# Optimization experiments

Measured on AMD Instinct MI355X. Metric: run time of the kernel, lower is better.

## Reference

```python
import jax, jax.numpy as jnp
import numpy as np

N = 65536      # total voxels (lidar + image tokens)
D = 256        # d_model
H = 8          # nhead
DFF = 2048     # dim_feedforward
SS = 128       # set_size
SN = 512       # set_num (SN * SS == N, each partition is a permutation of all voxels)
NSHIFT = 2


def setup_inputs() -> dict:
    key = jax.random.key(0)
    ks = jax.random.split(key, 10)
    src = jax.random.normal(ks[0], (N, D), jnp.float32)
    pos_embed = jax.random.normal(ks[1], (NSHIFT, N, D), jnp.float32) * 0.02
    # each (shift, set_id) partition covers every voxel exactly once
    inds = jnp.stack([
        jnp.stack([
            jax.random.permutation(jax.random.fold_in(ks[2], s * 2 + p), N).reshape(SN, SS)
            for p in range(2)
        ])
        for s in range(NSHIFT)
    ]).astype(jnp.int32)                      # (NSHIFT, 2, SN, SS)
    masks = jax.random.uniform(ks[3], (NSHIFT, 2, SN, SS)) < 0.1
    masks = masks.at[..., 0].set(False)       # keep at least one key per set
    init = lambda k, shape: jax.random.normal(k, shape, jnp.float32) * 0.02
    return {
        'src': src, 'pos_embed': pos_embed,
        'set_voxel_inds': inds, 'set_voxel_masks': masks,
        'w_qkv': init(ks[4], (2, 3 * D, D)), 'b_qkv': jnp.zeros((2, 3 * D)),
        'w_out': init(ks[5], (2, D, D)), 'b_out': jnp.zeros((2, D)),
        'w_ff1': init(ks[6], (2, DFF, D)), 'b_ff1': jnp.zeros((2, DFF)),
        'w_ff2': init(ks[7], (2, D, DFF)), 'b_ff2': jnp.zeros((2, D)),
        'g_n1': jnp.ones((2, D)), 'b_n1': jnp.zeros((2, D)),
        'g_n2': jnp.ones((2, D)), 'b_n2': jnp.zeros((2, D)),
        'g_ln': jnp.ones((2, D)), 'b_ln': jnp.zeros((2, D)),
    }


def _ln(x, g, b):
    m = jnp.mean(x, -1, keepdims=True)
    v = jnp.mean(jnp.square(x - m), -1, keepdims=True)
    return (x - m) * jax.lax.rsqrt(v + 1e-5) * g + b


def _mha(q_in, k_in, v_in, mask, wqkv, bqkv, wo, bo):
    # q_in/k_in/v_in: (SN, SS, D); mask: (SN, SS) True = ignore key
    wq, wk, wv = jnp.split(wqkv, 3, axis=0)
    bq, bk, bv = jnp.split(bqkv, 3, axis=0)
    hd = D // H
    q = (q_in @ wq.T + bq).reshape(SN, SS, H, hd)
    k = (k_in @ wk.T + bk).reshape(SN, SS, H, hd)
    v = (v_in @ wv.T + bv).reshape(SN, SS, H, hd)
    scores = jnp.einsum('bqhd,bkhd->bhqk', q, k) / np.float32(np.sqrt(hd))
    scores = jnp.where(mask[:, None, None, :], jnp.float32(-1e9), scores)
    attn = jax.nn.softmax(scores, axis=-1)
    o = jnp.einsum('bhqk,bkhd->bqhd', attn, v).reshape(SN, SS, D)
    return o @ wo.T + bo


def reference(src, pos_embed, set_voxel_inds, set_voxel_masks,
              w_qkv, b_qkv, w_out, b_out, w_ff1, b_ff1, w_ff2, b_ff2,
              g_n1, b_n1, g_n2, b_n2, g_ln, b_ln):
    out = src
    set_id = 0  # block_id % 2 with block_id == 0
    for i in range(NSHIFT):  # two encoder layers, one per shift
        inds = set_voxel_inds[i, set_id]   # (SN, SS)
        mask = set_voxel_masks[i, set_id]  # (SN, SS)
        pos = pos_embed[i]
        identity = out
        feat = out[inds]                   # gather voxels into sets
        qk = feat + pos[inds]
        a = _mha(qk, qk, feat, mask, w_qkv[i], b_qkv[i], w_out[i], b_out[i])
        # scatter back: per voxel, take its FIRST occurrence in flattened set order
        flat = inds.reshape(-1)
        L = flat.shape[0]
        perm = jnp.full((N,), L, jnp.int32).at[flat].min(jnp.arange(L, dtype=jnp.int32))
        src2 = a.reshape(-1, D)[perm]
        x = _ln(out + src2, g_n1[i], b_n1[i])
        ff = jax.nn.relu(x @ w_ff1[i].T + b_ff1[i]) @ w_ff2[i].T + b_ff2[i]
        x = _ln(x + ff, g_n2[i], b_n2[i])
        out = _ln(x + identity, g_ln[i], b_ln[i])
    return out
```

## Files before the change

kernel.cpp:

```cpp
#include <hip/hip_runtime.h>
#include <math.h>

#define NVOX 65536
#define DM 256
#define NH 8
#define HDIM 32
#define DFFN 2048
#define SSZ 128
#define SNUM 512

#define AS1 __attribute__((address_space(1)))
#define AS3 __attribute__((address_space(3)))

typedef __attribute__((ext_vector_type(8))) __bf16 bf16x8;
typedef __attribute__((ext_vector_type(8))) unsigned short u16x8;
typedef __attribute__((ext_vector_type(4))) float f32x4;

__device__ __forceinline__ unsigned short f2bf(float f) {
    unsigned int u = __float_as_uint(f);
    u += 0x7fffu + ((u >> 16) & 1u);
    return (unsigned short)(u >> 16);
}
__device__ __forceinline__ float bf2f(unsigned short u) {
    return __uint_as_float(((unsigned int)u) << 16);
}

__global__ __launch_bounds__(256)
void cvt_bf16_kernel(const float* __restrict__ in, unsigned short* __restrict__ out, int n) {
    int i = blockIdx.x * 256 + threadIdx.x;
    int stride = gridDim.x * 256;
    for (; i < n; i += stride) out[i] = f2bf(in[i]);
}

__global__ __launch_bounds__(256)
void gather_kernel(const float* __restrict__ src, const float* __restrict__ pos,
                   const int* __restrict__ inds,
                   unsigned short* __restrict__ qk, unsigned short* __restrict__ feat) {
    int j = blockIdx.x * 4 + (threadIdx.x >> 6);
    int lane = threadIdx.x & 63;
    int v = inds[j];
    float4 a = ((const float4*)(src + (size_t)v * DM))[lane];
    float4 p = ((const float4*)(pos + (size_t)v * DM))[lane];
    ushort4 qo, fo;
    qo.x = f2bf(a.x + p.x); qo.y = f2bf(a.y + p.y);
    qo.z = f2bf(a.z + p.z); qo.w = f2bf(a.w + p.w);
    fo.x = f2bf(a.x); fo.y = f2bf(a.y); fo.z = f2bf(a.z); fo.w = f2bf(a.w);
    ((ushort4*)(qk   + (size_t)j * DM))[lane] = qo;
    ((ushort4*)(feat + (size_t)j * DM))[lane] = fo;
}

#define VMCNT4 asm volatile("s_waitcnt vmcnt(4)" ::: "memory")
#define VMCNT0 asm volatile("s_waitcnt vmcnt(0)" ::: "memory")

template<int EPI, bool RELU>
__global__ __launch_bounds__(512)
void gemm_mfma256(const unsigned short* __restrict__ A, const unsigned short* __restrict__ W,
                  const float* __restrict__ bias, void* __restrict__ Cout,
                  int M, int N, int K,
                  const int* __restrict__ inds,
                  const float* __restrict__ res1, const float* __restrict__ res2,
                  const float* __restrict__ g1, const float* __restrict__ b1,
                  const float* __restrict__ g2, const float* __restrict__ b2,
                  unsigned short* __restrict__ out2) {
    __shared__ alignas(16) char smem[69632];
    unsigned short* As = (unsigned short*)smem;
    unsigned short* Bs = (unsigned short*)(smem + 32768);
    float* ebuf = (float*)smem;
    const int ES = 264;

    int tid = threadIdx.x;
    int wave = tid >> 6, lane = tid & 63;
    int wm = wave >> 2;
    int wn = wave & 3;

    unsigned lin = blockIdx.x + blockIdx.y * gridDim.x;
    unsigned nwg = gridDim.x * gridDim.y;
    unsigned swz = lin;
    if ((nwg & 7u) == 0u) { unsigned cpx = nwg >> 3; swz = (lin & 7u) * cpx + (lin >> 3); }
    int bx = (int)(swz / gridDim.y);
    int by = (int)(swz % gridDim.y);
    int mBase = bx * 256, nBase = by * 256;

    int rr = lane & 15;
    int kq = (lane >> 4) * 8;
    int rbase = (lane >> 4) * 4;

    f32x4 acc[8][4];
    const f32x4 zero = {0.f, 0.f, 0.f, 0.f};
#pragma unroll
    for (int m = 0; m < 8; m++)
#pragma unroll
        for (int n = 0; n < 4; n++) acc[m][n] = zero;

    const unsigned short* gA0 = A + (size_t)(mBase + (wave * 2 + 0) * 16 + rr) * K + kq;
    const unsigned short* gA1 = A + (size_t)(mBase + (wave * 2 + 1) * 16 + rr) * K + kq;
    const unsigned short* gB0 = W + (size_t)(nBase + (wave * 2 + 0) * 16 + rr) * K + kq;
    const unsigned short* gB1 = W + (size_t)(nBase + (wave * 2 + 1) * 16 + rr) * K + kq;

    auto stage = [&](int b, int kt) {
        int ko = kt * 32;
        __builtin_amdgcn_global_load_lds((const AS1 void*)(gA0 + ko),
            (AS3 void*)(As + b * 8192 + (wave * 2 + 0) * 512), 16, 0, 0);
        __builtin_amdgcn_global_load_lds((const AS1 void*)(gA1 + ko),
            (AS3 void*)(As + b * 8192 + (wave * 2 + 1) * 512), 16, 0, 0);
        __builtin_amdgcn_global_load_lds((const AS1 void*)(gB0 + ko),
            (AS3 void*)(Bs + b * 8192 + (wave * 2 + 0) * 512), 16, 0, 0);
        __builtin_amdgcn_global_load_lds((const AS1 void*)(gB1 + ko),
            (AS3 void*)(Bs + b * 8192 + (wave * 2 + 1) * 512), 16, 0, 0);
    };

    int nt = K >> 5;
    stage(0, 0);

    for (int t = 0; t < nt; ++t) {
        int p = t & 1;
        if (t + 1 < nt) {
            stage(p ^ 1, t + 1);
            VMCNT4;
        } else {
            VMCNT0;
        }
        __builtin_amdgcn_s_barrier();
        __builtin_amdgcn_sched_barrier(0);

        bf16x8 af[8], bf[4];
#pragma unroll
        for (int m = 0; m < 8; m++)
            af[m] = *(const bf16x8*)(As + p * 8192 + (wm * 8 + m) * 512 + lane * 8);
#pragma unroll
        for (int n = 0; n < 4; n++)
            bf[n] = *(const bf16x8*)(Bs + p * 8192 + (wn * 4 + n) * 512 + lane * 8);
#pragma unroll
        for (int m = 0; m < 8; m++)
#pragma unroll
            for (int n = 0; n < 4; n++)
                acc[m][n] = __builtin_amdgcn_mfma_f32_16x16x32_bf16(af[m], bf[n], acc[m][n], 0, 0, 0);

        __builtin_amdgcn_sched_barrier(0);
        __builtin_amdgcn_s_barrier();
    }

    float bn[4];
#pragma unroll
    for (int n = 0; n < 4; n++)
        bn[n] = bias[nBase + wn * 64 + n * 16 + rr];

    int erow = tid >> 3;
    int ec0  = (tid & 7) * 32;
#pragma unroll
    for (int pass = 0; pass < 4; ++pass) {
        __syncthreads();
        if (wm == (pass >> 1)) {
#pragma unroll
            for (int mm = 0; mm < 4; ++mm) {
                int m = (pass & 1) * 4 + mm;
#pragma unroll
                for (int n = 0; n < 4; ++n) {
                    int lcol = wn * 64 + n * 16 + rr;
#pragma unroll
                    for (int r = 0; r < 4; ++r) {
                        float v = acc[m][n][r] + bn[n];
                        if (RELU) v = fmaxf(v, 0.f);
                        ebuf[(mm * 16 + rbase + r) * ES + lcol] = v;
                    }
                }
            }
        }
        __syncthreads();
        int grow = mBase + pass * 64 + erow;

        if constexpr (EPI == 0) {
            unsigned short* dst = (unsigned short*)Cout + (size_t)grow * N + nBase + ec0;
#pragma unroll
            for (int g = 0; g < 4; ++g) {
                u16x8 o;
#pragma unroll
                for (int j = 0; j < 8; ++j)
                    o[j] = f2bf(ebuf[erow * ES + ec0 + g * 8 + j]);
                *(u16x8*)(dst + g * 8) = o;
            }
        } else if constexpr (EPI == 1) {
            float* dst = (float*)Cout + (size_t)grow * N + nBase + ec0;
#pragma unroll
            for (int g = 0; g < 8; ++g)
                *(float4*)(dst + g * 4) = *(float4*)(ebuf + erow * ES + ec0 + g * 4);
        } else if constexpr (EPI == 2) {
            int v = inds[grow];
            const float* pr = res1 + (size_t)v * 256;
            f32x4 tv[8];
            float s = 0.f, s2 = 0.f;
#pragma unroll
            for (int g = 0; g < 8; ++g) {
                float4 e = *(float4*)(ebuf + erow * ES + ec0 + g * 4);
                float4 p = *(const float4*)(pr + ec0 + g * 4);
                f32x4 t = {e.x + p.x, e.y + p.y, e.z + p.z, e.w + p.w};
                tv[g] = t;
                s += t[0] + t[1] + t[2] + t[3];
                s2 += t[0]*t[0] + t[1]*t[1] + t[2]*t[2] + t[3]*t[3];
            }
#pragma unroll
            for (int off = 1; off < 8; off <<= 1) { s += __shfl_xor(s, off); s2 += __shfl_xor(s2, off); }
            float mean = s * (1.f/256.f);
            float var = fmaf(-mean, mean, s2 * (1.f/256.f));
            float rs = rsqrtf(var + 1e-5f);
            float* xd = (float*)Cout + (size_t)v * 256 + ec0;
            unsigned short* xb = out2 + (size_t)v * 256 + ec0;
#pragma unroll
            for (int g = 0; g < 8; ++g) {
                float4 gg = *(const float4*)(g1 + ec0 + g * 4);
                float4 bb = *(const float4*)(b1 + ec0 + g * 4);
                float4 o;
                o.x = fmaf((tv[g][0] - mean) * rs, gg.x, bb.x);
                o.y = fmaf((tv[g][1] - mean) * rs, gg.y, bb.y);
                o.z = fmaf((tv[g][2] - mean) * rs, gg.z, bb.z);
                o.w = fmaf((tv[g][3] - mean) * rs, gg.w, bb.w);
                *(float4*)(xd + g * 4) = o;
                ushort4 ob; ob.x = f2bf(o.x); ob.y = f2bf(o.y); ob.z = f2bf(o.z); ob.w = f2bf(o.w);
                *(ushort4*)(xb + g * 4) = ob;
            }
        } else {
            const float* xr = res2 + (size_t)grow * 256;
            const float* pr = res1 + (size_t)grow * 256;
            f32x4 tv[8];
            float s = 0.f, s2 = 0.f;
#pragma unroll
            for (int g = 0; g < 8; ++g) {
                float4 e = *(float4*)(ebuf + erow * ES + ec0 + g * 4);
                float4 x = *(const float4*)(xr + ec0 + g * 4);
                f32x4 t = {e.x + x.x, e.y + x.y, e.z + x.z, e.w + x.w};
                tv[g] = t;
                s += t[0] + t[1] + t[2] + t[3];
                s2 += t[0]*t[0] + t[1]*t[1] + t[2]*t[2] + t[3]*t[3];
            }
#pragma unroll
            for (int off = 1; off < 8; off <<= 1) { s += __shfl_xor(s, off); s2 += __shfl_xor(s2, off); }
            float mean = s * (1.f/256.f);
            float var = fmaf(-mean, mean, s2 * (1.f/256.f));
            float rs = rsqrtf(var + 1e-5f);
            float s3 = 0.f, s4 = 0.f;
#pragma unroll
            for (int g = 0; g < 8; ++g) {
                float4 gg = *(const float4*)(g1 + ec0 + g * 4);
                float4 bb = *(const float4*)(b1 + ec0 + g * 4);
                float4 p = *(const float4*)(pr + ec0 + g * 4);
                f32x4 u;
                u[0] = fmaf((tv[g][0] - mean) * rs, gg.x, bb.x) + p.x;
                u[1] = fmaf((tv[g][1] - mean) * rs, gg.y, bb.y) + p.y;
                u[2] = fmaf((tv[g][2] - mean) * rs, gg.z, bb.z) + p.z;
                u[3] = fmaf((tv[g][3] - mean) * rs, gg.w, bb.w) + p.w;
                tv[g] = u;
                s3 += u[0] + u[1] + u[2] + u[3];
                s4 += u[0]*u[0] + u[1]*u[1] + u[2]*u[2] + u[3]*u[3];
            }
#pragma unroll
            for (int off = 1; off < 8; off <<= 1) { s3 += __shfl_xor(s3, off); s4 += __shfl_xor(s4, off); }
            float mean2 = s3 * (1.f/256.f);
            float var2 = fmaf(-mean2, mean2, s4 * (1.f/256.f));
            float rs2 = rsqrtf(var2 + 1e-5f);
            float* od = (float*)Cout + (size_t)grow * 256 + ec0;
#pragma unroll
            for (int g = 0; g < 8; ++g) {
                float4 gg = *(const float4*)(g2 + ec0 + g * 4);
                float4 bb = *(const float4*)(b2 + ec0 + g * 4);
                float4 o;
                o.x = fmaf((tv[g][0] - mean2) * rs2, gg.x, bb.x);
                o.y = fmaf((tv[g][1] - mean2) * rs2, gg.y, bb.y);
                o.z = fmaf((tv[g][2] - mean2) * rs2, gg.z, bb.z);
                o.w = fmaf((tv[g][3] - mean2) * rs2, gg.w, bb.w);
                *(float4*)(od + g * 4) = o;
            }
        }
    }
}

__global__ __launch_bounds__(256)
void attn_mfma_kernel(const unsigned short* __restrict__ QK,
                      const unsigned short* __restrict__ V,
                      const unsigned char* __restrict__ mask,
                      unsigned short* __restrict__ ao) {
    int s = blockIdx.x, h = blockIdx.y;
    int tid = threadIdx.x;
    int wq = tid >> 6;
    int lane = tid & 63;

    __shared__ alignas(16) unsigned short Ks[128 * 40];
    __shared__ alignas(16) unsigned short Vt[32 * 136];
    __shared__ alignas(16) unsigned short Plds[4 * 4096];
    __shared__ unsigned char msk[SSZ];

#pragma unroll
    for (int it = 0; it < 2; it++) {
        int idx = tid + it * 256;
        int key = idx >> 2, dimoff = (idx & 3) * 8;
        bf16x8 kv = *(const bf16x8*)(QK + (size_t)(s * SSZ + key) * 512 + 256 + h * HDIM + dimoff);
        *(bf16x8*)(Ks + key * 40 + dimoff) = kv;
        u16x8 vv = *(const u16x8*)(V + (size_t)(s * SSZ + key) * DM + h * HDIM + dimoff);
#pragma unroll
        for (int j = 0; j < 8; j++) Vt[(dimoff + j) * 136 + key] = vv[j];
    }
    if (tid < SSZ) msk[tid] = mask[s * SSZ + tid];
    __syncthreads();

    int rr = lane & 15;
    int kq = (lane >> 4) * 8;
    const f32x4 zero = {0.f, 0.f, 0.f, 0.f};

    bf16x8 qa[2];
#pragma unroll
    for (int mt = 0; mt < 2; mt++)
        qa[mt] = *(const bf16x8*)(QK + (size_t)(s * SSZ + wq * 32 + mt * 16 + rr) * 512 + h * HDIM + kq);

    f32x4 S[2][8];
#pragma unroll
    for (int nt = 0; nt < 8; nt++) {
        bf16x8 kb = *(const bf16x8*)(Ks + (nt * 16 + rr) * 40 + kq);
#pragma unroll
        for (int mt = 0; mt < 2; mt++)
            S[mt][nt] = __builtin_amdgcn_mfma_f32_16x16x32_bf16(qa[mt], kb, zero, 0, 0, 0);
    }

    const float SCALE = 0.17677669529663687f;
    f32x4 rm[2];
#pragma unroll
    for (int mt = 0; mt < 2; mt++) { rm[mt].x = rm[mt].y = rm[mt].z = rm[mt].w = -1e30f; }
#pragma unroll
    for (int nt = 0; nt < 8; nt++) {
        bool mv = msk[nt * 16 + rr] != 0;
#pragma unroll
        for (int mt = 0; mt < 2; mt++) {
#pragma unroll
            for (int r = 0; r < 4; r++) {
                float v = mv ? -1e30f : S[mt][nt][r] * SCALE;
                S[mt][nt][r] = v;
                rm[mt][r] = fmaxf(rm[mt][r], v);
            }
        }
    }
#pragma unroll
    for (int off = 1; off < 16; off <<= 1) {
#pragma unroll
        for (int mt = 0; mt < 2; mt++)
#pragma unroll
            for (int r = 0; r < 4; r++)
                rm[mt][r] = fmaxf(rm[mt][r], __shfl_xor(rm[mt][r], off));
    }

    f32x4 rs[2];
#pragma unroll
    for (int mt = 0; mt < 2; mt++) { rs[mt] = zero; }
#pragma unroll
    for (int nt = 0; nt < 8; nt++)
#pragma unroll
        for (int mt = 0; mt < 2; mt++)
#pragma unroll
            for (int r = 0; r < 4; r++) {
                float p = __expf(S[mt][nt][r] - rm[mt][r]);
                S[mt][nt][r] = p;
                rs[mt][r] += p;
            }
#pragma unroll
    for (int off = 1; off < 16; off <<= 1) {
#pragma unroll
        for (int mt = 0; mt < 2; mt++)
#pragma unroll
            for (int r = 0; r < 4; r++)
                rs[mt][r] += __shfl_xor(rs[mt][r], off);
    }

    char* Pbase = (char*)Plds + wq * 8192;
#pragma unroll
    for (int nt = 0; nt < 8; nt++)
#pragma unroll
        for (int mt = 0; mt < 2; mt++)
#pragma unroll
            for (int r = 0; r < 4; r++) {
                int prow = mt * 16 + (lane >> 4) * 4 + r;
                int col  = nt * 16 + rr;
                unsigned addr = (unsigned)(prow * 256 + col * 2) ^ ((prow & 7) << 4);
                *(unsigned short*)(Pbase + addr) = f2bf(S[mt][nt][r]);
            }
    __syncthreads();

    f32x4 O[2][2];
#pragma unroll
    for (int mt = 0; mt < 2; mt++)
#pragma unroll
        for (int nd = 0; nd < 2; nd++) O[mt][nd] = zero;
#pragma unroll
    for (int kc = 0; kc < 4; kc++) {
        bf16x8 pa[2];
#pragma unroll
        for (int mt = 0; mt < 2; mt++) {
            int prow = mt * 16 + rr;
            unsigned addr = (unsigned)(prow * 256 + (kc * 32 + kq) * 2) ^ ((prow & 7) << 4);
            pa[mt] = *(const bf16x8*)(Pbase + addr);
        }
#pragma unroll
        for (int nd = 0; nd < 2; nd++) {
            bf16x8 vb = *(const bf16x8*)(Vt + (nd * 16 + rr) * 136 + kc * 32 + kq);
#pragma unroll
            for (int mt = 0; mt < 2; mt++)
                O[mt][nd] = __builtin_amdgcn_mfma_f32_16x16x32_bf16(pa[mt], vb, O[mt][nd], 0, 0, 0);
        }
    }

#pragma unroll
    for (int mt = 0; mt < 2; mt++) {
#pragma unroll
        for (int nd = 0; nd < 2; nd++) {
#pragma unroll
            for (int r = 0; r < 4; r++) {
                int row = s * SSZ + wq * 32 + mt * 16 + (lane >> 4) * 4 + r;
                int col = h * HDIM + nd * 16 + rr;
                ao[(size_t)row * DM + col] = f2bf(O[mt][nd][r] / rs[mt][r]);
            }
        }
    }
}

extern "C" void kernel_launch(void* const* d_in, const int* in_sizes, int n_in,
                              void* d_out, int out_size, void* d_ws, size_t ws_size,
                              hipStream_t stream) {
    const float* src       = (const float*)d_in[0];
    const float* pos_embed = (const float*)d_in[1];
    const int*   inds_all  = (const int*)d_in[2];
    const unsigned char* masks_all = (const unsigned char*)d_in[3];
    const float* w_qkv = (const float*)d_in[4];
    const float* b_qkv = (const float*)d_in[5];
    const float* w_out = (const float*)d_in[6];
    const float* b_out = (const float*)d_in[7];
    const float* w_ff1 = (const float*)d_in[8];
    const float* b_ff1 = (const float*)d_in[9];
    const float* w_ff2 = (const float*)d_in[10];
    const float* b_ff2 = (const float*)d_in[11];
    const float* g_n1 = (const float*)d_in[12];
    const float* b_n1 = (const float*)d_in[13];
    const float* g_n2 = (const float*)d_in[14];
    const float* b_n2 = (const float*)d_in[15];
    const float* g_ln = (const float*)d_in[16];
    const float* b_ln = (const float*)d_in[17];
    float* out = (float*)d_out;

    const size_t NVF = (size_t)NVOX * DM;
    unsigned short* A = (unsigned short*)d_ws;
    unsigned short* B = A + NVF;
    unsigned short* C = B + NVF;
    unsigned short* D = C + 2 * NVF;
    float* F = (float*)(D + NVF);
    unsigned short* wts = (unsigned short*)(F + NVF);
    const size_t SZ_QKV = (size_t)2 * 3 * DM * DM;
    const size_t SZ_WO  = (size_t)2 * DM * DM;
    const size_t SZ_FF1 = (size_t)2 * DFFN * DM;
    const size_t SZ_FF2 = (size_t)2 * DM * DFFN;
    unsigned short* wqkv_bf = wts;
    unsigned short* wo_bf   = wqkv_bf + SZ_QKV;
    unsigned short* wff1_bf = wo_bf + SZ_WO;
    unsigned short* wff2_bf = wff1_bf + SZ_FF1;
    unsigned short* hbuf    = wff2_bf + SZ_FF2;

    size_t used_bytes = (char*)hbuf - (char*)d_ws;
    long long avail = (long long)ws_size - (long long)used_bytes;
    long long crows = avail / (DFFN * 2);
    if (crows > NVOX) crows = NVOX;
    crows &= ~2047LL;
    int chunk = (crows < 2048) ? 2048 : (int)crows;

    cvt_bf16_kernel<<<512, 256, 0, stream>>>(w_qkv, wqkv_bf, (int)SZ_QKV);
    cvt_bf16_kernel<<<256, 256, 0, stream>>>(w_out, wo_bf, (int)SZ_WO);
    cvt_bf16_kernel<<<1024, 256, 0, stream>>>(w_ff1, wff1_bf, (int)SZ_FF1);
    cvt_bf16_kernel<<<1024, 256, 0, stream>>>(w_ff2, wff2_bf, (int)SZ_FF2);

    for (int i = 0; i < 2; i++) {
        const float* prev = (i == 0) ? src : out;
        const int* inds = inds_all + (size_t)i * 2 * SNUM * SSZ;
        const unsigned char* mask = masks_all + (size_t)i * 2 * SNUM * SSZ;
        const float* pos  = pos_embed + (size_t)i * NVF;
        const unsigned short* wqkv = wqkv_bf + (size_t)i * 3 * DM * DM;
        const unsigned short* wo   = wo_bf + (size_t)i * DM * DM;
        const unsigned short* wff1 = wff1_bf + (size_t)i * DFFN * DM;
        const unsigned short* wff2 = wff2_bf + (size_t)i * DM * DFFN;
        const float* bqkv = b_qkv + (size_t)i * 3 * DM;
        const float* bo   = b_out + (size_t)i * DM;
        const float* bff1 = b_ff1 + (size_t)i * DFFN;
        const float* bff2 = b_ff2 + (size_t)i * DM;

        gather_kernel<<<NVOX / 4, 256, 0, stream>>>(prev, pos, inds, A, B);

        gemm_mfma256<0, false><<<dim3(NVOX / 256, 512 / 256), 512, 0, stream>>>(
            A, wqkv, bqkv, C, NVOX, 512, DM,
            nullptr, nullptr, nullptr, nullptr, nullptr, nullptr, nullptr, nullptr);
        gemm_mfma256<0, false><<<dim3(NVOX / 256, 1), 512, 0, stream>>>(
            B, wqkv + (size_t)512 * DM, bqkv + 512, D, NVOX, DM, DM,
            nullptr, nullptr, nullptr, nullptr, nullptr, nullptr, nullptr, nullptr);

        attn_mfma_kernel<<<dim3(SNUM, NH), 256, 0, stream>>>(C, D, mask, A);

        gemm_mfma256<2, false><<<dim3(NVOX / 256, 1), 512, 0, stream>>>(
            A, wo, bo, F, NVOX, DM, DM,
            inds, prev, nullptr, g_n1 + i * DM, b_n1 + i * DM, nullptr, nullptr, B);

        for (int r0 = 0; r0 < NVOX; r0 += chunk) {
            int rows = (NVOX - r0 < chunk) ? (NVOX - r0) : chunk;
            gemm_mfma256<0, true><<<dim3(rows / 256, DFFN / 256), 512, 0, stream>>>(
                B + (size_t)r0 * DM, wff1, bff1, hbuf, rows, DFFN, DM,
                nullptr, nullptr, nullptr, nullptr, nullptr, nullptr, nullptr, nullptr);
            gemm_mfma256<3, false><<<dim3(rows / 256, 1), 512, 0, stream>>>(
                hbuf, wff2, bff2, out + (size_t)r0 * DM, rows, DM, DFFN,
                nullptr, prev + (size_t)r0 * DM, F + (size_t)r0 * DM,
                g_n2 + i * DM, b_n2 + i * DM, g_ln + i * DM, b_ln + i * DM, nullptr);
        }
    }
}
```

Baseline: 1.173 ms.

## Fuse FFN1 and FFN2 into one kernel keeping hidden activations in LDS

Replaces the two FFN GEMM launches and the global hidden buffer with one kernel. For each 128-row tile it computes the hidden layer in 256-column chunks, applies bias and ReLU, stores the chunk as bf16 in swizzled LDS, and accumulates it straight into the output projection. The double layer-norm epilogue moves into this kernel. This removes the global write and read of the 65536x2048 bf16 hidden tensor, at the cost of smaller tiles, a large LDS footprint (120KB) and serialized per-chunk phases.

```diff
diff --git a/kernel.cpp b/kernel.cpp
--- a/kernel.cpp
+++ b/kernel.cpp
@@ -24,6 +24,12 @@
 __device__ __forceinline__ float bf2f(unsigned short u) {
     return __uint_as_float(((unsigned int)u) << 16);
 }
+
+#define VMCNT0 asm volatile("s_waitcnt vmcnt(0)" ::: "memory")
+#define VMCNT2 asm volatile("s_waitcnt vmcnt(2)" ::: "memory")
+#define VMCNT3 asm volatile("s_waitcnt vmcnt(3)" ::: "memory")
+#define VMCNT4 asm volatile("s_waitcnt vmcnt(4)" ::: "memory")
+#define LGKM0  asm volatile("s_waitcnt lgkmcnt(0)" ::: "memory")
 
 __global__ __launch_bounds__(256)
 void cvt_bf16_kernel(const float* __restrict__ in, unsigned short* __restrict__ out, int n) {
@@ -49,18 +55,14 @@
     ((ushort4*)(feat + (size_t)j * DM))[lane] = fo;
 }
 
-#define VMCNT4 asm volatile("s_waitcnt vmcnt(4)" ::: "memory")
-#define VMCNT0 asm volatile("s_waitcnt vmcnt(0)" ::: "memory")
-
 template<int EPI, bool RELU>
 __global__ __launch_bounds__(512)
 void gemm_mfma256(const unsigned short* __restrict__ A, const unsigned short* __restrict__ W,
                   const float* __restrict__ bias, void* __restrict__ Cout,
                   int M, int N, int K,
                   const int* __restrict__ inds,
-                  const float* __restrict__ res1, const float* __restrict__ res2,
+                  const float* __restrict__ res1,
                   const float* __restrict__ g1, const float* __restrict__ b1,
-                  const float* __restrict__ g2, const float* __restrict__ b2,
                   unsigned short* __restrict__ out2) {
     __shared__ alignas(16) char smem[69632];
     unsigned short* As = (unsigned short*)smem;
@@ -114,12 +116,8 @@
 
     for (int t = 0; t < nt; ++t) {
         int p = t & 1;
-        if (t + 1 < nt) {
-            stage(p ^ 1, t + 1);
-            VMCNT4;
-        } else {
-            VMCNT0;
-        }
+        if (t + 1 < nt) { stage(p ^ 1, t + 1); VMCNT4; }
+        else { VMCNT0; }
         __builtin_amdgcn_s_barrier();
         __builtin_amdgcn_sched_barrier(0);
 
@@ -179,12 +177,7 @@
                     o[j] = f2bf(ebuf[erow * ES + ec0 + g * 8 + j]);
                 *(u16x8*)(dst + g * 8) = o;
             }
-        } else if constexpr (EPI == 1) {
-            float* dst = (float*)Cout + (size_t)grow * N + nBase + ec0;
-#pragma unroll
-            for (int g = 0; g < 8; ++g)
-                *(float4*)(dst + g * 4) = *(float4*)(ebuf + erow * ES + ec0 + g * 4);
-        } else if constexpr (EPI == 2) {
+        } else {
             int v = inds[grow];
             const float* pr = res1 + (size_t)v * 256;
             f32x4 tv[8];
@@ -218,57 +211,217 @@
                 ushort4 ob; ob.x = f2bf(o.x); ob.y = f2bf(o.y); ob.z = f2bf(o.z); ob.w = f2bf(o.w);
                 *(ushort4*)(xb + g * 4) = ob;
             }
+        }
+    }
+}
+
+__global__ __launch_bounds__(512, 2)
+void ffn_fused(const unsigned short* __restrict__ X,
+               const unsigned short* __restrict__ W1,
+               const unsigned short* __restrict__ W2,
+               const float* __restrict__ b1g,
+               const float* __restrict__ b2g,
+               const float* __restrict__ xf,
+               const float* __restrict__ prev,
+               const float* __restrict__ lnG1, const float* __restrict__ lnB1,
+               const float* __restrict__ lnG2, const float* __restrict__ lnB2,
+               float* __restrict__ out) {
+    __shared__ alignas(16) char smem[122880];
+    unsigned short* Xbuf = (unsigned short*)smem;
+    unsigned short* Wbuf = (unsigned short*)(smem + 16384);
+    char*           HsB  = smem + 49152;
+    float*          B1s  = (float*)(smem + 114688);
+    float*          ebuf = (float*)smem;
+    const int ES = 264;
+
+    int tid = threadIdx.x;
+    int wave = tid >> 6, lane = tid & 63;
+    int wm = wave >> 2;
+    int wn = wave & 3;
+    int mBase = blockIdx.x * 128;
+    int rr = lane & 15;
+    int kq = (lane >> 4) * 8;
+    int rbase = (lane >> 4) * 4;
+
+    {
+        float4 bv = *(const float4*)(b1g + tid * 4);
+        *(float4*)(B1s + tid * 4) = bv;
+    }
+    __syncthreads();
+
+    auto gll = [&](const unsigned short* g, unsigned short* l) {
+        __builtin_amdgcn_global_load_lds((const AS1 void*)g, (AS3 void*)l, 16, 0, 0);
+    };
+    auto stage_slice = [&](int s) {
+        int c = s >> 4, half = (s >> 3) & 1, kt = s & 7;
+        unsigned short* wb = Wbuf + (s & 1) * 8192;
+        if (half == 0) {
+            gll(X + (size_t)(mBase + wave * 16 + rr) * 256 + kt * 32 + kq,
+                Xbuf + (kt & 1) * 4096 + wave * 512);
+            gll(W1 + (size_t)(c * 256 + (wave * 2 + 0) * 16 + rr) * 256 + kt * 32 + kq,
+                wb + (wave * 2 + 0) * 512);
+            gll(W1 + (size_t)(c * 256 + (wave * 2 + 1) * 16 + rr) * 256 + kt * 32 + kq,
+                wb + (wave * 2 + 1) * 512);
         } else {
-            const float* xr = res2 + (size_t)grow * 256;
-            const float* pr = res1 + (size_t)grow * 256;
-            f32x4 tv[8];
-            float s = 0.f, s2 = 0.f;
-#pragma unroll
-            for (int g = 0; g < 8; ++g) {
-                float4 e = *(float4*)(ebuf + erow * ES + ec0 + g * 4);
-                float4 x = *(const float4*)(xr + ec0 + g * 4);
-                f32x4 t = {e.x + x.x, e.y + x.y, e.z + x.z, e.w + x.w};
-                tv[g] = t;
-                s += t[0] + t[1] + t[2] + t[3];
-                s2 += t[0]*t[0] + t[1]*t[1] + t[2]*t[2] + t[3]*t[3];
-            }
-#pragma unroll
-            for (int off = 1; off < 8; off <<= 1) { s += __shfl_xor(s, off); s2 += __shfl_xor(s2, off); }
-            float mean = s * (1.f/256.f);
-            float var = fmaf(-mean, mean, s2 * (1.f/256.f));
-            float rs = rsqrtf(var + 1e-5f);
-            float s3 = 0.f, s4 = 0.f;
-#pragma unroll
-            for (int g = 0; g < 8; ++g) {
-                float4 gg = *(const float4*)(g1 + ec0 + g * 4);
-                float4 bb = *(const float4*)(b1 + ec0 + g * 4);
-                float4 p = *(const float4*)(pr + ec0 + g * 4);
-                f32x4 u;
-                u[0] = fmaf((tv[g][0] - mean) * rs, gg.x, bb.x) + p.x;
-                u[1] = fmaf((tv[g][1] - mean) * rs, gg.y, bb.y) + p.y;
-                u[2] = fmaf((tv[g][2] - mean) * rs, gg.z, bb.z) + p.z;
-                u[3] = fmaf((tv[g][3] - mean) * rs, gg.w, bb.w) + p.w;
-                tv[g] = u;
-                s3 += u[0] + u[1] + u[2] + u[3];
-                s4 += u[0]*u[0] + u[1]*u[1] + u[2]*u[2] + u[3]*u[3];
-            }
-#pragma unroll
-            for (int off = 1; off < 8; off <<= 1) { s3 += __shfl_xor(s3, off); s4 += __shfl_xor(s4, off); }
-            float mean2 = s3 * (1.f/256.f);
-            float var2 = fmaf(-mean2, mean2, s4 * (1.f/256.f));
-            float rs2 = rsqrtf(var2 + 1e-5f);
-            float* od = (float*)Cout + (size_t)grow * 256 + ec0;
-#pragma unroll
-            for (int g = 0; g < 8; ++g) {
-                float4 gg = *(const float4*)(g2 + ec0 + g * 4);
-                float4 bb = *(const float4*)(b2 + ec0 + g * 4);
-                float4 o;
-                o.x = fmaf((tv[g][0] - mean2) * rs2, gg.x, bb.x);
-                o.y = fmaf((tv[g][1] - mean2) * rs2, gg.y, bb.y);
-                o.z = fmaf((tv[g][2] - mean2) * rs2, gg.z, bb.z);
-                o.w = fmaf((tv[g][3] - mean2) * rs2, gg.w, bb.w);
-                *(float4*)(od + g * 4) = o;
-            }
+            gll(W2 + (size_t)((wave * 2 + 0) * 16 + rr) * 2048 + c * 256 + kt * 32 + kq,
+                wb + (wave * 2 + 0) * 512);
+            gll(W2 + (size_t)((wave * 2 + 1) * 16 + rr) * 2048 + c * 256 + kt * 32 + kq,
+                wb + (wave * 2 + 1) * 512);
+        }
+    };
+
+    f32x4 yacc[4][4];
+    const f32x4 zero = {0.f, 0.f, 0.f, 0.f};
+#pragma unroll
+    for (int m = 0; m < 4; m++)
+#pragma unroll
+        for (int n = 0; n < 4; n++) yacc[m][n] = zero;
+
+    stage_slice(0);
+
+    for (int c = 0; c < 8; ++c) {
+        f32x4 hacc[4][4];
+#pragma unroll
+        for (int m = 0; m < 4; m++)
+#pragma unroll
+            for (int n = 0; n < 4; n++) hacc[m][n] = zero;
+
+#pragma unroll
+        for (int kt = 0; kt < 8; ++kt) {
+            int s = c * 16 + kt;
+            stage_slice(s + 1);
+            if (kt < 7) VMCNT3; else VMCNT2;
+            __builtin_amdgcn_s_barrier();
+            __builtin_amdgcn_sched_barrier(0);
+
+            bf16x8 af[4], bf[4];
+#pragma unroll
+            for (int m = 0; m < 4; m++)
+                af[m] = *(const bf16x8*)(Xbuf + (kt & 1) * 4096 + (wm * 4 + m) * 512 + lane * 8);
+#pragma unroll
+            for (int n = 0; n < 4; n++)
+                bf[n] = *(const bf16x8*)(Wbuf + (s & 1) * 8192 + (wn * 4 + n) * 512 + lane * 8);
+#pragma unroll
+            for (int m = 0; m < 4; m++)
+#pragma unroll
+                for (int n = 0; n < 4; n++)
+                    hacc[m][n] = __builtin_amdgcn_mfma_f32_16x16x32_bf16(af[m], bf[n], hacc[m][n], 0, 0, 0);
+
+            __builtin_amdgcn_sched_barrier(0);
+            __builtin_amdgcn_s_barrier();
+        }
+
+        {
+            float b1v[4];
+#pragma unroll
+            for (int n = 0; n < 4; n++)
+                b1v[n] = B1s[c * 256 + wn * 64 + n * 16 + rr];
+#pragma unroll
+            for (int m = 0; m < 4; m++)
+#pragma unroll
+                for (int n = 0; n < 4; n++)
+#pragma unroll
+                    for (int r = 0; r < 4; r++) {
+                        float v = fmaxf(hacc[m][n][r] + b1v[n], 0.f);
+                        int row = wm * 64 + m * 16 + rbase + r;
+                        int col = wn * 64 + n * 16 + rr;
+                        unsigned byte = (unsigned)(row * 512 + col * 2) ^ ((row & 7) << 4);
+                        *(unsigned short*)(HsB + byte) = f2bf(v);
+                    }
+            LGKM0;
+            __builtin_amdgcn_s_barrier();
+        }
+
+#pragma unroll
+        for (int kt = 0; kt < 8; ++kt) {
+            int s = c * 16 + 8 + kt;
+            if (s + 1 < 128) stage_slice(s + 1);
+            if (s + 1 >= 128) { VMCNT0; }
+            else if (kt < 7) { VMCNT2; }
+            else { VMCNT3; }
+            __builtin_amdgcn_s_barrier();
+            __builtin_amdgcn_sched_barrier(0);
+
+            bf16x8 af[4], bf[4];
+#pragma unroll
+            for (int m = 0; m < 4; m++) {
+                int row = wm * 64 + m * 16 + rr;
+                unsigned byte = (unsigned)(row * 512 + kt * 64 + (lane >> 4) * 16) ^ ((rr & 7) << 4);
+                af[m] = *(const bf16x8*)(HsB + byte);
+            }
+#pragma unroll
+            for (int n = 0; n < 4; n++)
+                bf[n] = *(const bf16x8*)(Wbuf + (s & 1) * 8192 + (wn * 4 + n) * 512 + lane * 8);
+#pragma unroll
+            for (int m = 0; m < 4; m++)
+#pragma unroll
+                for (int n = 0; n < 4; n++)
+                    yacc[m][n] = __builtin_amdgcn_mfma_f32_16x16x32_bf16(af[m], bf[n], yacc[m][n], 0, 0, 0);
+
+            __builtin_amdgcn_sched_barrier(0);
+            __builtin_amdgcn_s_barrier();
+        }
+    }
+
+    float b2v[4];
+#pragma unroll
+    for (int n = 0; n < 4; n++)
+        b2v[n] = b2g[wn * 64 + n * 16 + rr];
+
+    int erow = tid >> 5;
+    int ec0  = (tid & 31) * 8;
+#pragma unroll
+    for (int p = 0; p < 8; ++p) {
+        __syncthreads();
+        if (wm == (p >> 2)) {
+            const int m = p & 3;
+#pragma unroll
+            for (int n = 0; n < 4; ++n) {
+                int lcol = wn * 64 + n * 16 + rr;
+#pragma unroll
+                for (int r = 0; r < 4; ++r)
+                    ebuf[(rbase + r) * ES + lcol] = yacc[m][n][r] + b2v[n];
+            }
+        }
+        __syncthreads();
+        int grow = mBase + p * 16 + erow;
+
+        float tv[8];
+        float s1 = 0.f, s2 = 0.f;
+        const float* xr = xf + (size_t)grow * 256 + ec0;
+#pragma unroll
+        for (int j = 0; j < 8; ++j) {
+            float t = ebuf[erow * ES + ec0 + j] + xr[j];
+            tv[j] = t; s1 += t; s2 += t * t;
+        }
+#pragma unroll
+        for (int off = 1; off < 32; off <<= 1) { s1 += __shfl_xor(s1, off); s2 += __shfl_xor(s2, off); }
+        float mean = s1 * (1.f/256.f);
+        float var = fmaf(-mean, mean, s2 * (1.f/256.f));
+        float rs = rsqrtf(var + 1e-5f);
+
+        const float* pr = prev + (size_t)grow * 256 + ec0;
+        float s3 = 0.f, s4 = 0.f;
+#pragma unroll
+        for (int j = 0; j < 8; ++j) {
+            float u = fmaf((tv[j] - mean) * rs, lnG1[ec0 + j], lnB1[ec0 + j]) + pr[j];
+            tv[j] = u; s3 += u; s4 += u * u;
+        }
+#pragma unroll
+        for (int off = 1; off < 32; off <<= 1) { s3 += __shfl_xor(s3, off); s4 += __shfl_xor(s4, off); }
+        float mean2 = s3 * (1.f/256.f);
+        float var2 = fmaf(-mean2, mean2, s4 * (1.f/256.f));
+        float rs2 = rsqrtf(var2 + 1e-5f);
+
+        float* od = out + (size_t)grow * 256 + ec0;
+#pragma unroll
+        for (int g = 0; g < 2; ++g) {
+            float4 o;
+            o.x = fmaf((tv[g*4+0] - mean2) * rs2, lnG2[ec0 + g*4+0], lnB2[ec0 + g*4+0]);
+            o.y = fmaf((tv[g*4+1] - mean2) * rs2, lnG2[ec0 + g*4+1], lnB2[ec0 + g*4+1]);
+            o.z = fmaf((tv[g*4+2] - mean2) * rs2, lnG2[ec0 + g*4+2], lnB2[ec0 + g*4+2]);
+            o.w = fmaf((tv[g*4+3] - mean2) * rs2, lnG2[ec0 + g*4+3], lnB2[ec0 + g*4+3]);
+            *(float4*)(od + g * 4) = o;
         }
     }
 }
@@ -456,14 +609,6 @@
     unsigned short* wo_bf   = wqkv_bf + SZ_QKV;
     unsigned short* wff1_bf = wo_bf + SZ_WO;
     unsigned short* wff2_bf = wff1_bf + SZ_FF1;
-    unsigned short* hbuf    = wff2_bf + SZ_FF2;
-
-    size_t used_bytes = (char*)hbuf - (char*)d_ws;
-    long long avail = (long long)ws_size - (long long)used_bytes;
-    long long crows = avail / (DFFN * 2);
-    if (crows > NVOX) crows = NVOX;
-    crows &= ~2047LL;
-    int chunk = (crows < 2048) ? 2048 : (int)crows;
 
     cvt_bf16_kernel<<<512, 256, 0, stream>>>(w_qkv, wqkv_bf, (int)SZ_QKV);
     cvt_bf16_kernel<<<256, 256, 0, stream>>>(w_out, wo_bf, (int)SZ_WO);
@@ -488,26 +633,19 @@
 
         gemm_mfma256<0, false><<<dim3(NVOX / 256, 512 / 256), 512, 0, stream>>>(
             A, wqkv, bqkv, C, NVOX, 512, DM,
-            nullptr, nullptr, nullptr, nullptr, nullptr, nullptr, nullptr, nullptr);
+            nullptr, nullptr, nullptr, nullptr, nullptr);
         gemm_mfma256<0, false><<<dim3(NVOX / 256, 1), 512, 0, stream>>>(
             B, wqkv + (size_t)512 * DM, bqkv + 512, D, NVOX, DM, DM,
-            nullptr, nullptr, nullptr, nullptr, nullptr, nullptr, nullptr, nullptr);
+            nullptr, nullptr, nullptr, nullptr, nullptr);
 
         attn_mfma_kernel<<<dim3(SNUM, NH), 256, 0, stream>>>(C, D, mask, A);
 
         gemm_mfma256<2, false><<<dim3(NVOX / 256, 1), 512, 0, stream>>>(
             A, wo, bo, F, NVOX, DM, DM,
-            inds, prev, nullptr, g_n1 + i * DM, b_n1 + i * DM, nullptr, nullptr, B);
-
-        for (int r0 = 0; r0 < NVOX; r0 += chunk) {
-            int rows = (NVOX - r0 < chunk) ? (NVOX - r0) : chunk;
-            gemm_mfma256<0, true><<<dim3(rows / 256, DFFN / 256), 512, 0, stream>>>(
-                B + (size_t)r0 * DM, wff1, bff1, hbuf, rows, DFFN, DM,
-                nullptr, nullptr, nullptr, nullptr, nullptr, nullptr, nullptr, nullptr);
-            gemm_mfma256<3, false><<<dim3(rows / 256, 1), 512, 0, stream>>>(
-                hbuf, wff2, bff2, out + (size_t)r0 * DM, rows, DM, DFFN,
-                nullptr, prev + (size_t)r0 * DM, F + (size_t)r0 * DM,
-                g_n2 + i * DM, b_n2 + i * DM, g_ln + i * DM, b_ln + i * DM, nullptr);
-        }
-    }
-}
+            inds, prev, g_n1 + i * DM, b_n1 + i * DM, B);
+
+        ffn_fused<<<dim3(NVOX / 128), 512, 0, stream>>>(
+            B, wff1, wff2, bff1, bff2, F, prev,
+            g_n2 + i * DM, b_n2 + i * DM, g_ln + i * DM, b_ln + i * DM, out);
+    }
+}
```

New measurement: 1.118 ms. 4.7% less time.
